# Kernel optimization log

Hardware: AMD Instinct MI355X
Metric: run time of the kernel (lower is better)

Reference implementation:

```python
import jax, jax.numpy as jnp
import numpy as np

PAD = -999.0       # PADDING_INDEX (float coords)
PAD_I = -999       # PADDING_INDEX (int seq)
EPS = 1e-12        # clamp epsilon in scoreDistro
N_ID, CA_ID, C_ID = 0, 1, 2  # at_name encoding for backbone atoms


def setup_inputs() -> dict:
    nb, mc, mr, nalt = 64, 4, 2048, 2
    n_res_types = 20
    nres = nb * mc * mr
    rng = np.random.default_rng(0)
    # 4 atoms per residue: N, CA, C, O
    batch = np.repeat(np.arange(nb), mc * mr * 4)
    chain = np.tile(np.repeat(np.arange(mc), mr * 4), nb)
    resnum = np.tile(np.repeat(np.arange(mr), 4), nb * mc)
    resname = np.repeat(rng.integers(0, n_res_types, nres), 4)
    atname = np.tile(np.array([0, 1, 2, 3]), nres)
    ad = np.stack([batch, chain, resnum, resname, atname], 1).astype(np.int64)
    coords = (rng.standard_normal((nres * 4, 3)) * 5.0).astype(np.float32)
    alternatives = np.ones((nres * 4, nalt), dtype=bool)
    mean = (np.array([1.33, 2.1, 2.0], np.float32)
            + 0.05 * rng.standard_normal((n_res_types, 3))).astype(np.float32)
    std = (0.02 + 0.08 * rng.random((n_res_types, 3))).astype(np.float32)
    weight = np.array([-5.0], np.float32)
    return {
        'atom_description': jnp.asarray(ad),
        'coords': jnp.asarray(coords),
        'alternatives': jnp.asarray(alternatives),
        'mean': jnp.asarray(mean),
        'std': jnp.asarray(std),
        'weight': jnp.asarray(weight),
        'nbatch': nb, 'maxchain': mc, 'maxres': mr,
    }


def _angle(v1, v2):
    # math_utils.angle2dVectors: angle between vectors, radians
    n1 = jnp.linalg.norm(v1, axis=-1)
    n2 = jnp.linalg.norm(v2, axis=-1)
    cos = jnp.sum(v1 * v2, axis=-1) / jnp.maximum(n1 * n2, 1e-12)
    return jnp.arccos(jnp.clip(cos, -1.0 + 1e-7, 1.0 - 1e-7))


def reference(atom_description, coords, alternatives, mean, std, weight,
              nbatch, maxchain, maxres):
    batch = atom_description[:, 0]
    chain = atom_description[:, 1]
    resnum = atom_description[:, 2]
    resname = atom_description[:, 3]
    atname = atom_description[:, 4]
    nalt = alternatives.shape[-1]

    def scatter(mask, vals, fill, trail):
        # index_put_ equivalent; masked-out atoms routed out-of-bounds -> dropped
        b = jnp.where(mask, batch, nbatch)
        out = jnp.full((nbatch, maxchain, maxres) + trail, fill, vals.dtype)
        return out.at[b, chain, resnum].set(vals, mode='drop')

    Narr = scatter(atname == N_ID, coords, PAD, (3,))
    Carr = scatter(atname == C_ID, coords, PAD, (3,))
    CAarr = scatter(atname == CA_ID, coords, PAD, (3,))
    seq = scatter(atname == CA_ID, resname, PAD_I, ())

    # gather bonded atoms: residue i (next) and residue i-1 (prev)
    N_next = Narr[:, :, 1:]    # [nb, mc, mr-1, 3]
    C_prev = Carr[:, :, :-1]
    CA_next = CAarr[:, :, 1:]
    CA_prev = CAarr[:, :, :-1]

    pad_mask = (seq[:, :, 1:] != PAD_I) & (seq[:, :, :-1] != PAD_I)
    present = lambda x: x[..., 0] != PAD
    todo = (present(N_next) & present(C_prev) & present(CA_next)
            & present(CA_prev) & pad_mask)

    bond_len = jnp.linalg.norm(N_next - C_prev, axis=-1)
    c_n_ca = _angle(C_prev - N_next, CA_next - N_next)
    ca_c_n = _angle(CA_prev - C_prev, N_next - C_prev)
    feats = jnp.stack([bond_len, c_n_ca, ca_c_n], axis=-1)  # [nb,mc,mr-1,3]

    # scoreDistro: per-dim Gaussian negative log-likelihood (vectorized over dims)
    sidx = jnp.where(todo, seq[:, :, 1:], 0)
    mu = mean[sidx]                          # [nb,mc,mr-1,3]
    var = std[sidx] ** 2
    denom = jnp.sqrt(2.0 * jnp.pi * var)
    num = jnp.exp(-(feats - mu) ** 2 / (2.0 * var))
    score = -(jnp.log(jnp.maximum(num / denom, EPS)) - jnp.log(1.0 / denom))
    scores = score.sum(-1) * (1.0 - jnp.tanh(-weight[0]))

    e = jnp.where(todo, scores, 0.0)         # [nb,mc,mr-1]
    # per-alt results are identical (single-id atom sets make the alt mask a no-op)
    resiEnergy = jnp.zeros((nbatch, maxchain, maxres, nalt), jnp.float32)
    resiEnergy = resiEnergy.at[:, :, 1:, :].set(
        jnp.broadcast_to(e[..., None], e.shape + (nalt,)))
    return resiEnergy
```

## Files before the change

### kernel.cpp

```cpp
#include <hip/hip_runtime.h>
#include <math.h>


#define MAX_RT 128

typedef float vf4 __attribute__((ext_vector_type(4)));
typedef float vf2 __attribute__((ext_vector_type(2)));
typedef int   vi4 __attribute__((ext_vector_type(4)));

__device__ __forceinline__ float angle3(float v1x, float v1y, float v1z,
                                        float v2x, float v2y, float v2z) {
    float n1 = sqrtf(v1x*v1x + v1y*v1y + v1z*v1z);
    float n2 = sqrtf(v2x*v2x + v2y*v2y + v2z*v2z);
    float cc = (v1x*v2x + v1y*v2y + v1z*v2z) / fmaxf(n1 * n2, 1e-12f);
    cc = fminf(fmaxf(cc, -1.0f + 1e-07f), 1.0f - 1e-07f);
    return acosf(cc);
}

__global__ __launch_bounds__(256) void fused_kernel(
        const int*   __restrict__ ad,
        const float* __restrict__ coords,
        const float* __restrict__ mean,
        const float* __restrict__ stdv,
        const float* __restrict__ weight,
        const int*   __restrict__ mr_p,
        float*       __restrict__ out,
        int nslots, int nalt, int nrt) {

    __shared__ float s_c[3084];
    __shared__ float s_mu[3*MAX_RT], s_inv2v[3*MAX_RT], s_cut[3*MAX_RT];
    __shared__ float s_ws;

    const int tid = threadIdx.x;
    const int s0  = blockIdx.x * 256;
    const int s   = s0 + tid;

    int rn = 0;
    if (s < nslots) {
        const vi4* a4 = reinterpret_cast<const vi4*>(ad);
        vi4 t = __builtin_nontemporal_load(a4 + (size_t)5 * s);
        rn = t.w;
    }
    const int mr = *mr_p;

    for (int k = tid; k < 3*nrt; k += 256) {
        float sd   = stdv[k];
        s_mu[k]    = mean[k];
        s_inv2v[k] = 1.0f / (2.0f * sd * sd);
        s_cut[k]   = 26.7120825827f - logf(sd);
    }
    if (tid == 0) s_ws = 1.0f - tanhf(-weight[0]);

    {
        const vf4* c4   = reinterpret_cast<const vf4*>(coords);
        vf4*       sc4  = reinterpret_cast<vf4*>(s_c);
        const int  b4   = 3 * (s0 - 1);
        const int  lim4 = 3 * nslots;
        #pragma unroll
        for (int g = tid; g < 771; g += 256) {
            int G = b4 + g;
            if (G >= 0 && G < lim4)
                sc4[g] = __builtin_nontemporal_load(c4 + G);
        }
    }
    __syncthreads();

    if (s >= nslots) return;

    const int rres = ((mr & (mr - 1)) == 0) ? (s & (mr - 1)) : (s % mr);

    float e = 0.0f;
    if (rres != 0) {
        const int lr = tid + 1;
        float Nx = s_c[lr*12 + 0], Ny = s_c[lr*12 + 1], Nz = s_c[lr*12 + 2];
        float Ax = s_c[lr*12 + 3], Ay = s_c[lr*12 + 4], Az = s_c[lr*12 + 5];
        float Px = s_c[lr*12 - 9], Py = s_c[lr*12 - 8], Pz = s_c[lr*12 - 7];
        float Cx = s_c[lr*12 - 6], Cy = s_c[lr*12 - 5], Cz = s_c[lr*12 - 4];

        int sidx = rn;
        if (sidx < 0) sidx = 0;
        if (sidx >= nrt) sidx = nrt - 1;
        const int kb = 3 * sidx;

        float dx = Nx - Cx, dy = Ny - Cy, dz = Nz - Cz;
        float bond_len = sqrtf(dx*dx + dy*dy + dz*dz);
        float a1 = angle3(Cx - Nx, Cy - Ny, Cz - Nz,
                          Ax - Nx, Ay - Ny, Az - Nz);
        float a2 = angle3(Px - Cx, Py - Cy, Pz - Cz,
                          Nx - Cx, Ny - Cy, Nz - Cz);

        float f0 = bond_len - s_mu[kb + 0];
        float f1 = a1       - s_mu[kb + 1];
        float f2 = a2       - s_mu[kb + 2];
        float score = fminf(f0*f0*s_inv2v[kb+0], s_cut[kb+0])
                    + fminf(f1*f1*s_inv2v[kb+1], s_cut[kb+1])
                    + fminf(f2*f2*s_inv2v[kb+2], s_cut[kb+2]);
        e = score * s_ws;
    }

    if (nalt == 2) {
        vf2 o; o.x = e; o.y = e;
        __builtin_nontemporal_store(o, reinterpret_cast<vf2*>(out) + s);
    } else {
        for (int a = 0; a < nalt; ++a) out[(size_t)s * nalt + a] = e;
    }
}

extern "C" void kernel_launch(void* const* d_in, const int* in_sizes, int n_in,
                              void* d_out, int out_size, void* d_ws, size_t ws_size,
                              hipStream_t stream) {
    const int*   ad     = (const int*)  d_in[0];
    const float* coords = (const float*)d_in[1];
    const float* mean   = (const float*)d_in[3];
    const float* stdv   = (const float*)d_in[4];
    const float* weight = (const float*)d_in[5];
    const int*   mr_p   = (const int*)  d_in[8];

    const int natoms = in_sizes[0] / 5;
    const int nalt   = in_sizes[2] / natoms;
    const int nslots = out_size / nalt;
    const int nrt    = in_sizes[3] / 3;

    const int B = 256;
    fused_kernel<<<(nslots + B - 1) / B, B, 0, stream>>>(
        ad, coords, mean, stdv, weight, mr_p,
        (float*)d_out, nslots, nalt, nrt);
}
```

Before: 16.25 us.

## Use per-wave coordinate staging and direct parameter loads instead of block sync

Each 64-lane wave now stages its own coordinate window in a private LDS slice and synchronises with a wave barrier instead of a block-wide __syncthreads. The shared-memory tables of Gaussian parameters are dropped. Each thread instead reads mean and std from global memory (through the cache) and computes the division, log and tanh inline. This removes the block barrier and the table setup phase. In exchange it adds redundant halo loads per wave and more per-thread transcendental work and global gathers.

```diff
diff --git a/kernel.cpp b/kernel.cpp
--- a/kernel.cpp
+++ b/kernel.cpp
@@ -1,8 +1,6 @@
 #include <hip/hip_runtime.h>
 #include <math.h>
 
-
-#define MAX_RT 128
 
 typedef float vf4 __attribute__((ext_vector_type(4)));
 typedef float vf2 __attribute__((ext_vector_type(2)));
@@ -27,13 +25,13 @@
         float*       __restrict__ out,
         int nslots, int nalt, int nrt) {
 
-    __shared__ float s_c[3084];
-    __shared__ float s_mu[3*MAX_RT], s_inv2v[3*MAX_RT], s_cut[3*MAX_RT];
-    __shared__ float s_ws;
+    __shared__ float s_c[4][780];
 
     const int tid = threadIdx.x;
-    const int s0  = blockIdx.x * 256;
-    const int s   = s0 + tid;
+    const int w   = tid >> 6;
+    const int l   = tid & 63;
+    const int sw  = blockIdx.x * 256 + w * 64;
+    const int s   = sw + l;
 
     int rn = 0;
     if (s < nslots) {
@@ -43,27 +41,28 @@
     }
     const int mr = *mr_p;
 
-    for (int k = tid; k < 3*nrt; k += 256) {
-        float sd   = stdv[k];
-        s_mu[k]    = mean[k];
-        s_inv2v[k] = 1.0f / (2.0f * sd * sd);
-        s_cut[k]   = 26.7120825827f - logf(sd);
-    }
-    if (tid == 0) s_ws = 1.0f - tanhf(-weight[0]);
-
     {
         const vf4* c4   = reinterpret_cast<const vf4*>(coords);
-        vf4*       sc4  = reinterpret_cast<vf4*>(s_c);
-        const int  b4   = 3 * (s0 - 1);
+        vf4*       sc4  = reinterpret_cast<vf4*>(s_c[w]);
+        const int  b4   = 3 * (sw - 1);
         const int  lim4 = 3 * nslots;
-        #pragma unroll
-        for (int g = tid; g < 771; g += 256) {
-            int G = b4 + g;
-            if (G >= 0 && G < lim4)
-                sc4[g] = __builtin_nontemporal_load(c4 + G);
+
+        int G0 = b4 + l;
+        if (G0 >= 0 && G0 < lim4)
+            sc4[l] = __builtin_nontemporal_load(c4 + G0);
+        int G1 = b4 + l + 64;
+        if (G1 < lim4)
+            sc4[l + 64] = __builtin_nontemporal_load(c4 + G1);
+        int G2 = b4 + l + 128;
+        if (G2 < lim4)
+            sc4[l + 128] = __builtin_nontemporal_load(c4 + G2);
+        if (l < 3) {
+            int G3 = b4 + l + 192;
+            if (G3 < lim4)
+                sc4[l + 192] = __builtin_nontemporal_load(c4 + G3);
         }
     }
-    __syncthreads();
+    __builtin_amdgcn_wave_barrier();
 
     if (s >= nslots) return;
 
@@ -71,11 +70,12 @@
 
     float e = 0.0f;
     if (rres != 0) {
-        const int lr = tid + 1;
-        float Nx = s_c[lr*12 + 0], Ny = s_c[lr*12 + 1], Nz = s_c[lr*12 + 2];
-        float Ax = s_c[lr*12 + 3], Ay = s_c[lr*12 + 4], Az = s_c[lr*12 + 5];
-        float Px = s_c[lr*12 - 9], Py = s_c[lr*12 - 8], Pz = s_c[lr*12 - 7];
-        float Cx = s_c[lr*12 - 6], Cy = s_c[lr*12 - 5], Cz = s_c[lr*12 - 4];
+        const float* sc = s_c[w];
+        const int base = (l + 1) * 12;
+        float Nx = sc[base + 0], Ny = sc[base + 1], Nz = sc[base + 2];
+        float Ax = sc[base + 3], Ay = sc[base + 4], Az = sc[base + 5];
+        float Px = sc[base - 9], Py = sc[base - 8], Pz = sc[base - 7];
+        float Cx = sc[base - 6], Cy = sc[base - 5], Cz = sc[base - 4];
 
         int sidx = rn;
         if (sidx < 0) sidx = 0;
@@ -89,13 +89,18 @@
         float a2 = angle3(Px - Cx, Py - Cy, Pz - Cz,
                           Nx - Cx, Ny - Cy, Nz - Cz);
 
-        float f0 = bond_len - s_mu[kb + 0];
-        float f1 = a1       - s_mu[kb + 1];
-        float f2 = a2       - s_mu[kb + 2];
-        float score = fminf(f0*f0*s_inv2v[kb+0], s_cut[kb+0])
-                    + fminf(f1*f1*s_inv2v[kb+1], s_cut[kb+1])
-                    + fminf(f2*f2*s_inv2v[kb+2], s_cut[kb+2]);
-        e = score * s_ws;
+        const float f[3] = {bond_len, a1, a2};
+        float score = 0.0f;
+        #pragma unroll
+        for (int k = 0; k < 3; ++k) {
+            const float mu = mean[kb + k];
+            const float sd = stdv[kb + k];
+            const float dd = f[k] - mu;
+            const float z  = (dd * dd) / (2.0f * sd * sd);
+            const float cut = 26.7120825827f - __logf(sd);
+            score += fminf(z, cut);
+        }
+        e = score * (1.0f - tanhf(-weight[0]));
     }
 
     if (nalt == 2) {
```

Measured after the change: 17.16 us. 1.06x slower.
